# Performance work log

Hardware: AMD Instinct MI355X
Metric: run time of the kernel (lower is better)

## Reference

```python
import jax, jax.numpy as jnp
import numpy as np

# (C,H,W) of x0..x11; flattened size +1 homogeneous coordinate per key
SHAPES = [(3,32,32),(96,32,32),(96,32,32),(96,16,16),(192,16,16),(192,16,16),(192,8,8),(192,8,8),(192,8,8),(640,1,1),(100,1,1),(10,1,1)]
# (Cin,Cout,k,stride,pad) for conv1..conv9
CONV = [(3,96,3,1,1),(96,96,3,1,1),(96,96,3,2,1),(96,192,3,1,1),(192,192,3,1,1),(192,192,3,2,1),(192,192,3,1,1),(192,192,1,1,0),(192,10,1,1,0)]
B = 128


def setup_inputs():
    key = jax.random.key(0)
    inp = {}
    k, key = jax.random.split(key)
    inp['x0'] = jax.random.normal(k, (int(np.prod(SHAPES[0])) + 1, B), jnp.float32)
    for i, s in enumerate(SHAPES):
        n = int(np.prod(s)) + 1
        k1, k2, key = jax.random.split(key, 3)
        inp['perm%d' % i] = jax.random.permutation(k1, n)
        inp['diag%d' % i] = jax.random.uniform(k2, (n,), jnp.float32, 0.5, 1.5)
    for j, (ci, co, ks, st, pd) in enumerate(CONV):
        k1, k2, key = jax.random.split(key, 3)
        inp['w%d' % (j + 1)] = jax.random.normal(k1, (co, ci, ks, ks), jnp.float32) / np.float32(np.sqrt(ci * ks * ks))
        inp['b%d' % (j + 1)] = jax.random.normal(k2, (co,), jnp.float32) * 0.01
    k1, k2, k3, k4 = jax.random.split(key, 4)
    inp['fw1'] = jax.random.normal(k1, (100, 640), jnp.float32) / np.float32(np.sqrt(640))
    inp['fb1'] = jax.random.normal(k2, (100,), jnp.float32) * 0.01
    inp['fw2'] = jax.random.normal(k3, (10, 100), jnp.float32) / np.float32(np.sqrt(100))
    inp['fb2'] = jax.random.normal(k4, (10,), jnp.float32) * 0.01
    return inp


def _decode(x, perm, diag):
    # A_inv @ x with A_inv = P^T D^{-1}; P^T gather index is argsort(perm)
    return (x / diag[:, None])[jnp.argsort(perm)]


def _encode(y, perm, diag):
    # A @ y with A = D P; (P y)[i] = y[perm[i]]
    return diag[:, None] * y[perm]


def _conv_aug(v, w, b, shape_in, stride, pad):
    # affine-augmented conv: [W b; 0 1] applied to [feat; t]
    C, H, Wd = shape_in
    feat, t = v[:-1], v[-1]                      # (C*H*W, B), (B,)
    x = feat.T.reshape(-1, C, H, Wd)
    y = jax.lax.conv_general_dilated(x, w, (stride, stride), [(pad, pad), (pad, pad)],
                                     dimension_numbers=('NCHW', 'OIHW', 'NCHW'))
    y = y + b[None, :, None, None] * t[:, None, None, None]
    yf = y.reshape(y.shape[0], -1).T             # (N_out, B)
    return jnp.concatenate([yf, t[None, :]], axis=0)


def _fc_aug(v, w, b):
    feat, t = v[:-1], v[-1]
    return jnp.concatenate([w @ feat + b[:, None] * t[None, :], t[None, :]], axis=0)


def _forward(x0, perms, diags, ws, bs, fw1, fb1, fw2, fb2):
    x = x0
    for i in range(9):
        v = _decode(x, perms[i], diags[i])
        y = _conv_aug(v, ws[i], bs[i], SHAPES[i], CONV[i][3], CONV[i][4])
        x = jax.nn.relu(_encode(y, perms[i + 1], diags[i + 1]))
    v = _decode(x, perms[9], diags[9])
    x = jax.nn.relu(_encode(_fc_aug(v, fw1, fb1), perms[10], diags[10]))
    v = _decode(x, perms[10], diags[10])
    return _encode(_fc_aug(v, fw2, fb2), perms[11], diags[11])


def reference(x0, perm0, perm1, perm2, perm3, perm4, perm5, perm6, perm7, perm8, perm9, perm10, perm11,
              diag0, diag1, diag2, diag3, diag4, diag5, diag6, diag7, diag8, diag9, diag10, diag11,
              w1, b1, w2, b2, w3, b3, w4, b4, w5, b5, w6, b6, w7, b7, w8, b8, w9, b9,
              fw1, fb1, fw2, fb2):
    perms = [perm0, perm1, perm2, perm3, perm4, perm5, perm6, perm7, perm8, perm9, perm10, perm11]
    diags = [diag0, diag1, diag2, diag3, diag4, diag5, diag6, diag7, diag8, diag9, diag10, diag11]
    ws = [w1, w2, w3, w4, w5, w6, w7, w8, w9]
    bs = [b1, b2, b3, b4, b5, b6, b7, b8, b9]
    return _forward(x0, perms, diags, ws, bs, fw1, fb1, fw2, fb2)
```

## Files before the change

kernel.cpp:

```cpp
#include <hip/hip_runtime.h>
#include <stdint.h>


#define B 128
#define ZPAD 2048
#define NBLK 1024
#define NTHR 256
#define JSTRIDE ((NBLK >> 3) * 4)
#define LEAFN (NBLK >> 3)
#define AGT __HIP_MEMORY_SCOPE_AGENT

typedef _Float16 f16_t;
typedef __attribute__((ext_vector_type(8))) _Float16 f16x8;
typedef __attribute__((ext_vector_type(4))) _Float16 f16x4;
typedef __attribute__((ext_vector_type(4))) float f32x4;

struct WArgs {
    const float* w[9]; const float* b[9];
    int Ci[9], Co[9], KS[9], Cp[9], NCG[9];
    int woff[10]; int boff[10];
};

struct Bufs {
    f16_t *x8in, *S0, *S1, *S2, *S3, *S4, *S5, *S6, *S7, *wp;
    float *bp, *bufA, *bufB, *tph;
    int* bar;
};

__device__ __forceinline__ void st_wt_u64(void* p, uint64_t v) {
    __hip_atomic_store((uint64_t*)p, v, __ATOMIC_RELAXED, AGT);
}
__device__ __forceinline__ void st_wt_u16(void* p, uint16_t v) {
    __hip_atomic_store((uint16_t*)p, v, __ATOMIC_RELAXED, AGT);
}
__device__ __forceinline__ void st_wt_f32(float* p, float v) {
    __hip_atomic_store(p, v, __ATOMIC_RELAXED, AGT);
}
__device__ __forceinline__ void st_wt_h(f16_t* p, f16_t v) {
    union { f16_t h; uint16_t u; } c; c.h = v;
    st_wt_u16(p, c.u);
}

__device__ __forceinline__ void gbar(int* bar, int ph) {
    asm volatile("s_waitcnt vmcnt(0)" ::: "memory");
    __syncthreads();
    if (threadIdx.x == 0) {
        int* leaf  = bar + (blockIdx.x & 7) * 32;
        int* ldone = bar + 256 + (blockIdx.x & 7) * 32;
        int* root  = bar + 512;
        int old = __hip_atomic_fetch_add(leaf, 1, __ATOMIC_RELAXED, AGT);
        if (old == (ph + 1) * LEAFN - 1) {
            __hip_atomic_fetch_add(root, 1, __ATOMIC_RELAXED, AGT);
            while (__hip_atomic_load(root, __ATOMIC_RELAXED, AGT) < (ph + 1) * 8)
                __builtin_amdgcn_s_sleep(8);
            __hip_atomic_store(ldone, ph + 1, __ATOMIC_RELAXED, AGT);
        } else {
            while (__hip_atomic_load(ldone, __ATOMIC_RELAXED, AGT) < ph + 1)
                __builtin_amdgcn_s_sleep(8);
        }
    }
    __syncthreads();
}

__device__ void prep_phase(const WArgs& A, const Bufs& Bf,
                           const float* __restrict__ x0, const int* __restrict__ perm0,
                           const float* __restrict__ diag0) {
    const int NT = NBLK * NTHR;
    const int gtid = blockIdx.x * NTHR + threadIdx.x;
    if (gtid < 512) {
        st_wt_u64((uint64_t*)Bf.x8in + gtid, 0ull);
        st_wt_u64((uint64_t*)Bf.S0 + gtid, 0ull);
        st_wt_u64((uint64_t*)Bf.S1 + gtid, 0ull);
        st_wt_u64((uint64_t*)Bf.S2 + gtid, 0ull);
        st_wt_u64((uint64_t*)Bf.S3 + gtid, 0ull);
        st_wt_u64((uint64_t*)Bf.S4 + gtid, 0ull);
        st_wt_u64((uint64_t*)Bf.S5 + gtid, 0ull);
        st_wt_u64((uint64_t*)Bf.S6 + gtid, 0ull);
        st_wt_u64((uint64_t*)Bf.S7 + gtid, 0ull);
    }
    if (gtid < 1024 * 128) {
        int p = gtid >> 7, n = gtid & 127;
        f16_t* base = Bf.x8in + ZPAD + p * 1024 + n * 8;
        st_wt_u16(base + 3, 0);
        st_wt_u64(base + 4, 0ull);
    }
    if (gtid < A.boff[9]) {
        int l = 0;
        while (gtid >= A.boff[l + 1]) ++l;
        int co = gtid - A.boff[l];
        st_wt_f32(Bf.bp + gtid, (co < A.Co[l]) ? A.b[l][co] : 0.f);
    }
    for (int idx = gtid; idx < A.woff[9]; idx += NT) {
        int l = 0;
        while (idx >= A.woff[l + 1]) ++l;
        int e = idx - A.woff[l];
        int j = e & 7;
        int t1_ = e >> 3;
        int Cp = A.Cp[l];
        int co = t1_ % Cp;
        int gg = t1_ / Cp;
        int ncg = A.NCG[l];
        int tap = gg / ncg, cg = gg - tap * ncg;
        int ks = A.KS[l];
        int kh = tap / ks, kw = tap - kh * ks;
        int ci = cg * 8 + j;
        float val = 0.f;
        if (co < A.Co[l] && tap < ks * ks && ci < A.Ci[l])
            val = A.w[l][(((size_t)co * A.Ci[l] + ci) * ks + kh) * ks + kw];
        st_wt_h(Bf.wp + idx, (f16_t)val);
    }
    for (int idx = gtid; idx < 3073 * B; idx += NT) {
        int row = idx >> 7, n = idx & 127;
        int i = perm0[row];
        float val = x0[(size_t)row * B + n] / diag0[row];
        if (i < 3072) {
            int c = i >> 10, pp = i & 1023;
            st_wt_h(Bf.x8in + ZPAD + pp * 1024 + n * 8 + c, (f16_t)val);
        } else {
            st_wt_f32(Bf.tph + n, val);
        }
    }
}

template <int KS, int NS, int NSPLIT, int CB, bool F32OUT,
          int Hi, int Wo_log2, int HWo, int STRD, int PAD,
          int NCG, int NCHUNK, int KGR, int Co, int Cp>
__device__ __forceinline__ void conv_layer(
    const f16_t* __restrict__ xin, const float* __restrict__ t_in,
    const f16_t* __restrict__ wp, const float* __restrict__ bp,
    f16_t* __restrict__ xout, float* __restrict__ t_out, float* __restrict__ f32out)
{
    constexpr int PF = 2;
    constexpr int MS = 4;
    constexpr int Wi = Hi;
    constexpr int PB8 = HWo / 8;
    constexpr int UJ = NSPLIT * CB * PB8;
    constexpr int HiWi = Hi * Wi;
    constexpr int HiWi4 = 4 * HiWi;
    constexpr int NCGHW = NCG * HiWi;
    const int wv = threadIdx.x >> 6;
    const int lane = threadIdx.x & 63;
    const int q = lane >> 4;
    const int r = lane & 15;
    const int X = blockIdx.x & 7;

    if (blockIdx.x == 0 && threadIdx.x < B) {
        float tvv = fmaxf(t_in[threadIdx.x], 0.f);
        if (F32OUT) st_wt_f32(f32out + (size_t)Co * HWo * B + threadIdx.x, tvv);
        else        st_wt_f32(t_out + threadIdx.x, tvv);
    }

    for (int j = (blockIdx.x >> 3) * 4 + wv; j < UJ; j += JSTRIDE) {
        int nh = 0, j2 = j;
        if (NSPLIT > 1) { nh = j % NSPLIT; j2 = j / NSPLIT; }
        const int cog = (CB > 1) ? (j2 % CB) : 0;
        const int jp  = (CB > 1) ? (j2 / CB) : j2;
        const int p = X * PB8 + jp;
        const int co0 = cog * 64;
        const int ncol0 = nh * (NS * 16);
        const int ncol8 = ncol0 * 8;
        const int ho = p >> Wo_log2;
        const int wo = p & ((1 << Wo_log2) - 1);
        const f16_t* xdata = xin + ZPAD;

        float tv[NS];
#pragma unroll
        for (int ns = 0; ns < NS; ++ns) tv[ns] = t_in[ncol0 + ns * 16 + r];

        f32x4 acc[MS][NS];
#pragma unroll
        for (int ms = 0; ms < MS; ++ms) {
            float4 b4 = *(const float4*)(bp + co0 + ms * 16 + q * 4);
#pragma unroll
            for (int ns = 0; ns < NS; ++ns) {
                acc[ms][ns][0] = b4.x * tv[ns];
                acc[ms][ns][1] = b4.y * tv[ns];
                acc[ms][ns][2] = b4.z * tv[ns];
                acc[ms][ns][3] = b4.w * tv[ns];
            }
        }

        const int hb = ho * STRD - PAD, wb = wo * STRD - PAD;
        const int wend = wb + KS;

        int g = q, cg = q, hi = hb, wi = wb, cgHW;
        {
            while (cg >= NCG) { cg -= NCG; ++wi; if (wi == wend) { wi = wb; ++hi; } }
            cgHW = cg * HiWi;
        }

        f16x8 bf[PF][NS], af[PF][MS];

        auto advance = [&]() {
            g += 4; cg += 4; cgHW += HiWi4;
            if constexpr (NCG >= 4) {
                int c2 = cg - NCG;
                bool wrap = c2 >= 0;
                int wn = wi + 1;
                bool ww = wrap & (wn == wend);
                cg   = wrap ? c2 : cg;
                cgHW = wrap ? cgHW - NCGHW : cgHW;
                wi   = wrap ? (ww ? wb : wn) : wi;
                hi   = ww ? hi + 1 : hi;
            } else {
                while (cg >= NCG) { cg -= NCG; cgHW -= NCGHW; ++wi; if (wi == wend) { wi = wb; ++hi; } }
            }
        };
        auto loadB = [&](f16x8* bb8) {
            bool v = (g < KGR) & ((unsigned)hi < (unsigned)Hi) & ((unsigned)wi < (unsigned)Wi);
            int boff = (cgHW + hi * Wi + wi) << 10;
            const f16_t* bb = xdata + (v ? boff : -ZPAD) + ncol8 + r * 8;
#pragma unroll
            for (int ns = 0; ns < NS; ++ns) bb8[ns] = *(const f16x8*)(bb + ns * 128);
        };
        auto loadA = [&](f16x8* a, int c) {
            int ac = c < NCHUNK ? c : NCHUNK - 1;
            const f16_t* ap = wp + (((ac * 4 + q) * Cp) + co0 + r) * 8;
#pragma unroll
            for (int ms = 0; ms < MS; ++ms) a[ms] = *(const f16x8*)(ap + ms * 128);
        };
        auto domfma = [&](f16x8* a, f16x8* bb8) {
#pragma unroll
            for (int ms = 0; ms < MS; ++ms)
#pragma unroll
                for (int ns = 0; ns < NS; ++ns)
                    acc[ms][ns] = __builtin_amdgcn_mfma_f32_16x16x32_f16(a[ms], bb8[ns], acc[ms][ns], 0, 0, 0);
        };

#pragma unroll
        for (int pf = 0; pf < PF; ++pf) { loadB(bf[pf]); loadA(af[pf], pf); advance(); }
        constexpr int nck = ((NCHUNK + PF - 1) / PF) * PF;
        for (int c = 0; c < nck; c += PF) {
#pragma unroll
            for (int pf = 0; pf < PF; ++pf) {
                domfma(af[pf], bf[pf]);
                loadB(bf[pf]); loadA(af[pf], c + PF + pf); advance();
            }
        }

        if constexpr (!F32OUT) {
#pragma unroll
            for (int ms = 0; ms < MS; ++ms) {
                int cob = co0 + ms * 16 + q * 4;
                if (cob < Co) {
                    int off0 = ((cob >> 3) * HWo + p) * 1024 + (cob & 7) + ncol8 + r * 8;
#pragma unroll
                    for (int ns = 0; ns < NS; ++ns) {
                        union { f16x4 h; uint64_t u; } cu;
                        cu.h[0] = (f16_t)fmaxf(acc[ms][ns][0], 0.f);
                        cu.h[1] = (f16_t)fmaxf(acc[ms][ns][1], 0.f);
                        cu.h[2] = (f16_t)fmaxf(acc[ms][ns][2], 0.f);
                        cu.h[3] = (f16_t)fmaxf(acc[ms][ns][3], 0.f);
                        st_wt_u64(xout + ZPAD + off0 + ns * 128, cu.u);
                    }
                }
            }
        } else {
#pragma unroll
            for (int ms = 0; ms < MS; ++ms)
#pragma unroll
                for (int ns = 0; ns < NS; ++ns)
#pragma unroll
                    for (int e = 0; e < 4; ++e) {
                        int co = co0 + ms * 16 + q * 4 + e;
                        if (co < Co)
                            st_wt_f32(f32out + ((size_t)co * HWo + p) * B + ncol0 + ns * 16 + r,
                                      fmaxf(acc[ms][ns][e], 0.f));
                    }
        }
    }
}

__device__ __forceinline__ void fc1_phase(const float* __restrict__ v, const float* __restrict__ w,
                                          const float* __restrict__ b, float* __restrict__ y,
                                          float* __restrict__ red) {
    int r = blockIdx.x;
    int n = threadIdx.x & 127;
    int kh = threadIdx.x >> 7;
    float t = v[640 * B + n];
    float a0 = 0.f, a1 = 0.f, a2 = 0.f, a3 = 0.f;
    float a4 = 0.f, a5 = 0.f, a6 = 0.f, a7 = 0.f;
    if (r != 100) {
        const float* wr = w + (size_t)r * 640 + kh * 320;
        const float* vr = v + (size_t)kh * 320 * B + n;
        for (int k = 0; k < 320; k += 8) {
            float4 w0 = *(const float4*)(wr + k);
            float4 w1 = *(const float4*)(wr + k + 4);
            a0 = fmaf(w0.x, vr[(k + 0) * B], a0);
            a1 = fmaf(w0.y, vr[(k + 1) * B], a1);
            a2 = fmaf(w0.z, vr[(k + 2) * B], a2);
            a3 = fmaf(w0.w, vr[(k + 3) * B], a3);
            a4 = fmaf(w1.x, vr[(k + 4) * B], a4);
            a5 = fmaf(w1.y, vr[(k + 5) * B], a5);
            a6 = fmaf(w1.z, vr[(k + 6) * B], a6);
            a7 = fmaf(w1.w, vr[(k + 7) * B], a7);
        }
    }
    float part = ((a0 + a1) + (a2 + a3)) + ((a4 + a5) + (a6 + a7));
    if (kh) red[n] = part;
    __syncthreads();
    if (!kh) {
        float val = (r == 100) ? t : b[r] * t + part + red[n];
        st_wt_f32(y + (size_t)r * B + n, fmaxf(val, 0.f));
    }
}

__device__ __forceinline__ void fc2_phase(const float* __restrict__ v, const float* __restrict__ w,
                                          const float* __restrict__ b, const int* __restrict__ perm,
                                          const float* __restrict__ diag, float* __restrict__ out) {
    if (threadIdx.x >= B) return;
    int jrow = blockIdx.x;
    int n = threadIdx.x;
    int r = perm[jrow];
    float d = diag[jrow];
    float t = v[100 * B + n];
    float val;
    if (r == 10) {
        val = t;
    } else {
        float a0 = 0.f, a1 = 0.f, a2 = 0.f, a3 = 0.f;
        const float* wr = w + (size_t)r * 100;
        for (int k = 0; k < 100; k += 4) {
            float4 w4 = *(const float4*)(wr + k);
            a0 = fmaf(w4.x, v[(size_t)(k + 0) * B + n], a0);
            a1 = fmaf(w4.y, v[(size_t)(k + 1) * B + n], a1);
            a2 = fmaf(w4.z, v[(size_t)(k + 2) * B + n], a2);
            a3 = fmaf(w4.w, v[(size_t)(k + 3) * B + n], a3);
        }
        val = b[r] * t + (a0 + a1) + (a2 + a3);
    }
    out[(size_t)jrow * B + n] = d * val;
}

__global__ __launch_bounds__(NTHR, 4) void meganet_kernel(
    WArgs A, Bufs Bf,
    const float* __restrict__ x0, const int* __restrict__ perm0, const float* __restrict__ diag0,
    const int* __restrict__ perm11, const float* __restrict__ diag11,
    const float* __restrict__ fw1, const float* __restrict__ fb1,
    const float* __restrict__ fw2, const float* __restrict__ fb2,
    float* __restrict__ out)
{
    __shared__ float red[128];
    int* bar = Bf.bar;
    float* tp = Bf.tph;

    prep_phase(A, Bf, x0, perm0, diag0);
    gbar(bar, 0);
    conv_layer<3, 2, 4, 2, false, 32, 5, 1024, 1, 1,  1,  3,   9,  96, 128>(
        Bf.x8in, tp, Bf.wp + A.woff[0], Bf.bp + A.boff[0], Bf.S0, tp + 128, nullptr);
    gbar(bar, 1);
    conv_layer<3, 2, 4, 2, false, 32, 5, 1024, 1, 1, 12, 27, 108,  96, 128>(
        Bf.S0, tp + 128, Bf.wp + A.woff[1], Bf.bp + A.boff[1], Bf.S1, tp + 256, nullptr);
    gbar(bar, 2);
    conv_layer<3, 1, 8, 2, false, 32, 4,  256, 2, 1, 12, 27, 108,  96, 128>(
        Bf.S1, tp + 256, Bf.wp + A.woff[2], Bf.bp + A.boff[2], Bf.S2, tp + 384, nullptr);
    gbar(bar, 3);
    conv_layer<3, 2, 4, 3, false, 16, 4,  256, 1, 1, 12, 27, 108, 192, 192>(
        Bf.S2, tp + 384, Bf.wp + A.woff[3], Bf.bp + A.boff[3], Bf.S3, tp + 512, nullptr);
    gbar(bar, 4);
    conv_layer<3, 2, 4, 3, false, 16, 4,  256, 1, 1, 24, 54, 216, 192, 192>(
        Bf.S3, tp + 512, Bf.wp + A.woff[4], Bf.bp + A.boff[4], Bf.S4, tp + 640, nullptr);
    gbar(bar, 5);
    conv_layer<3, 1, 8, 3, false, 16, 3,   64, 2, 1, 24, 54, 216, 192, 192>(
        Bf.S4, tp + 640, Bf.wp + A.woff[5], Bf.bp + A.boff[5], Bf.S5, tp + 768, nullptr);
    gbar(bar, 6);
    conv_layer<3, 1, 8, 3, false,  8, 3,   64, 1, 1, 24, 54, 216, 192, 192>(
        Bf.S5, tp + 768, Bf.wp + A.woff[6], Bf.bp + A.boff[6], Bf.S6, tp + 896, nullptr);
    gbar(bar, 7);
    conv_layer<1, 1, 8, 3, false,  8, 3,   64, 1, 0, 24,  6,  24, 192, 192>(
        Bf.S6, tp + 896, Bf.wp + A.woff[7], Bf.bp + A.boff[7], Bf.S7, tp + 1024, nullptr);
    gbar(bar, 8);
    conv_layer<1, 1, 8, 1, true,   8, 3,   64, 1, 0, 24,  6,  24,  10,  64>(
        Bf.S7, tp + 1024, Bf.wp + A.woff[8], Bf.bp + A.boff[8], nullptr, nullptr, Bf.bufA);
    gbar(bar, 9);
    if (blockIdx.x <= 100) fc1_phase(Bf.bufA, fw1, fb1, Bf.bufB, red);
    gbar(bar, 10);
    if (blockIdx.x < 11) fc2_phase(Bf.bufB, fw2, fb2, perm11, diag11, out);
}


extern "C" void kernel_launch(void* const* d_in, const int* in_sizes, int n_in,
                              void* d_out, int out_size, void* d_ws, size_t ws_size,
                              hipStream_t stream) {
    const float* x0 = (const float*)d_in[0];
    const int*   perm[12];
    const float* diag[12];
    for (int i = 0; i < 12; ++i) {
        perm[i] = (const int*)d_in[1 + 2 * i];
        diag[i] = (const float*)d_in[2 + 2 * i];
    }
    const float* wts[9];
    const float* bia[9];
    for (int j = 0; j < 9; ++j) {
        wts[j] = (const float*)d_in[25 + 2 * j];
        bia[j] = (const float*)d_in[26 + 2 * j];
    }
    const float* fw1 = (const float*)d_in[43];
    const float* fb1 = (const float*)d_in[44];
    const float* fw2 = (const float*)d_in[45];
    const float* fb2 = (const float*)d_in[46];
    float* out = (float*)d_out;

    static const int CiA[9]  = {3, 96, 96, 96, 192, 192, 192, 192, 192};
    static const int CoA[9]  = {96, 96, 96, 192, 192, 192, 192, 192, 10};
    static const int KSA[9]  = {3, 3, 3, 3, 3, 3, 3, 1, 1};
    static const int CpA[9]  = {128, 128, 128, 192, 192, 192, 192, 192, 64};
    static const int NCGA[9] = {1, 12, 12, 12, 24, 24, 24, 24, 24};
    static const int NCHK[9] = {3, 27, 27, 27, 54, 54, 54, 6, 6};

    char* p = (char*)d_ws;
    auto take = [&](size_t bytes) { char* q = p; p += (bytes + 4095) & ~(size_t)4095; return q; };
    Bufs Bf;
    Bf.x8in = (f16_t*)take((ZPAD + 1024 * 1024) * 2);
    Bf.S0   = (f16_t*)take((ZPAD + 12 * 1024 * 1024) * 2);
    Bf.S1   = (f16_t*)take((ZPAD + 12 * 1024 * 1024) * 2);
    Bf.S2   = (f16_t*)take((ZPAD + 3 * 1024 * 1024) * 2);
    Bf.S3   = (f16_t*)take((ZPAD + 6 * 1024 * 1024) * 2);
    Bf.S4   = (f16_t*)take((ZPAD + 6 * 1024 * 1024) * 2);
    Bf.S5   = (f16_t*)take((ZPAD + 1536 * 1024) * 2);
    Bf.S6   = (f16_t*)take((ZPAD + 1536 * 1024) * 2);
    Bf.S7   = (f16_t*)take((ZPAD + 1536 * 1024) * 2);
    Bf.wp   = (f16_t*)take(2888704);
    Bf.bp   = (float*)take(8192);
    Bf.bufA = (float*)take(641 * 128 * 4);
    Bf.bufB = (float*)take(101 * 128 * 4);
    Bf.tph  = (float*)take(10 * 128 * 4);
    Bf.bar  = (int*)  take(4096);

    WArgs WA;
    int wo = 0, bo = 0;
    for (int l = 0; l < 9; ++l) {
        WA.w[l] = wts[l]; WA.b[l] = bia[l];
        WA.Ci[l] = CiA[l]; WA.Co[l] = CoA[l]; WA.KS[l] = KSA[l];
        WA.Cp[l] = CpA[l]; WA.NCG[l] = NCGA[l];
        WA.woff[l] = wo; wo += NCHK[l] * 4 * CpA[l] * 8;
        WA.boff[l] = bo; bo += CpA[l];
    }
    WA.woff[9] = wo; WA.boff[9] = bo;

    hipMemsetAsync(Bf.bar, 0, 4096, stream);

    meganet_kernel<<<NBLK, NTHR, 0, stream>>>(
        WA, Bf, x0, perm[0], diag[0], perm[11], diag[11],
        fw1, fb1, fw2, fb2, out);
}
```

Before: 379.4 us.

## Shrink conv warp tile to one N-subtile and deepen activation prefetch queue

Each wave now computes a 64x16 output tile (NS=1) instead of 64x32 in the layers that used NS=2, with the batch split across 8 wave tasks in every layer. The B-operand loads now run through an 8-deep register ring, and the weight fragments use a separate 2-deep ring, replacing the old 2-stage prefetch. The aim is to keep more global loads in flight and to spread the work across more tasks so latency is hidden better. The cost is that each weight fragment is reused half as much, so more weight loads and more per-task index overhead are issued overall.

```diff
diff --git a/kernel.cpp b/kernel.cpp
--- a/kernel.cpp
+++ b/kernel.cpp
@@ -122,7 +122,7 @@
     }
 }
 
-template <int KS, int NS, int NSPLIT, int CB, bool F32OUT,
+template <int KS, int NSPLIT, int CB, bool F32OUT,
           int Hi, int Wo_log2, int HWo, int STRD, int PAD,
           int NCG, int NCHUNK, int KGR, int Co, int Cp>
 __device__ __forceinline__ void conv_layer(
@@ -130,7 +130,7 @@
     const f16_t* __restrict__ wp, const float* __restrict__ bp,
     f16_t* __restrict__ xout, float* __restrict__ t_out, float* __restrict__ f32out)
 {
-    constexpr int PF = 2;
+    constexpr int BD = 8;
     constexpr int MS = 4;
     constexpr int Wi = Hi;
     constexpr int PB8 = HWo / 8;
@@ -151,33 +151,28 @@
     }
 
     for (int j = (blockIdx.x >> 3) * 4 + wv; j < UJ; j += JSTRIDE) {
-        int nh = 0, j2 = j;
-        if (NSPLIT > 1) { nh = j % NSPLIT; j2 = j / NSPLIT; }
+        const int nh = j % NSPLIT;
+        const int j2 = j / NSPLIT;
         const int cog = (CB > 1) ? (j2 % CB) : 0;
         const int jp  = (CB > 1) ? (j2 / CB) : j2;
         const int p = X * PB8 + jp;
         const int co0 = cog * 64;
-        const int ncol0 = nh * (NS * 16);
+        const int ncol0 = nh * 16;
         const int ncol8 = ncol0 * 8;
         const int ho = p >> Wo_log2;
         const int wo = p & ((1 << Wo_log2) - 1);
         const f16_t* xdata = xin + ZPAD;
 
-        float tv[NS];
-#pragma unroll
-        for (int ns = 0; ns < NS; ++ns) tv[ns] = t_in[ncol0 + ns * 16 + r];
-
-        f32x4 acc[MS][NS];
+        const float tv = t_in[ncol0 + r];
+
+        f32x4 acc[MS];
 #pragma unroll
         for (int ms = 0; ms < MS; ++ms) {
             float4 b4 = *(const float4*)(bp + co0 + ms * 16 + q * 4);
-#pragma unroll
-            for (int ns = 0; ns < NS; ++ns) {
-                acc[ms][ns][0] = b4.x * tv[ns];
-                acc[ms][ns][1] = b4.y * tv[ns];
-                acc[ms][ns][2] = b4.z * tv[ns];
-                acc[ms][ns][3] = b4.w * tv[ns];
-            }
+            acc[ms][0] = b4.x * tv;
+            acc[ms][1] = b4.y * tv;
+            acc[ms][2] = b4.z * tv;
+            acc[ms][3] = b4.w * tv;
         }
 
         const int hb = ho * STRD - PAD, wb = wo * STRD - PAD;
@@ -189,7 +184,7 @@
             cgHW = cg * HiWi;
         }
 
-        f16x8 bf[PF][NS], af[PF][MS];
+        f16x8 bfq[BD], afq[2][MS];
 
         auto advance = [&]() {
             g += 4; cg += 4; cgHW += HiWi4;
@@ -206,12 +201,10 @@
                 while (cg >= NCG) { cg -= NCG; cgHW -= NCGHW; ++wi; if (wi == wend) { wi = wb; ++hi; } }
             }
         };
-        auto loadB = [&](f16x8* bb8) {
+        auto loadB = [&](f16x8& bb8) {
             bool v = (g < KGR) & ((unsigned)hi < (unsigned)Hi) & ((unsigned)wi < (unsigned)Wi);
             int boff = (cgHW + hi * Wi + wi) << 10;
-            const f16_t* bb = xdata + (v ? boff : -ZPAD) + ncol8 + r * 8;
-#pragma unroll
-            for (int ns = 0; ns < NS; ++ns) bb8[ns] = *(const f16x8*)(bb + ns * 128);
+            bb8 = *(const f16x8*)(xdata + (v ? boff : -ZPAD) + ncol8 + r * 8);
         };
         auto loadA = [&](f16x8* a, int c) {
             int ac = c < NCHUNK ? c : NCHUNK - 1;
@@ -219,22 +212,23 @@
 #pragma unroll
             for (int ms = 0; ms < MS; ++ms) a[ms] = *(const f16x8*)(ap + ms * 128);
         };
-        auto domfma = [&](f16x8* a, f16x8* bb8) {
+        auto domfma = [&](f16x8* a, f16x8 bv) {
 #pragma unroll
             for (int ms = 0; ms < MS; ++ms)
-#pragma unroll
-                for (int ns = 0; ns < NS; ++ns)
-                    acc[ms][ns] = __builtin_amdgcn_mfma_f32_16x16x32_f16(a[ms], bb8[ns], acc[ms][ns], 0, 0, 0);
+                acc[ms] = __builtin_amdgcn_mfma_f32_16x16x32_f16(a[ms], bv, acc[ms], 0, 0, 0);
         };
 
 #pragma unroll
-        for (int pf = 0; pf < PF; ++pf) { loadB(bf[pf]); loadA(af[pf], pf); advance(); }
-        constexpr int nck = ((NCHUNK + PF - 1) / PF) * PF;
-        for (int c = 0; c < nck; c += PF) {
-#pragma unroll
-            for (int pf = 0; pf < PF; ++pf) {
-                domfma(af[pf], bf[pf]);
-                loadB(bf[pf]); loadA(af[pf], c + PF + pf); advance();
+        for (int pf = 0; pf < BD; ++pf) { loadB(bfq[pf]); advance(); }
+        loadA(afq[0], 0);
+        loadA(afq[1], 1);
+        constexpr int nck = ((NCHUNK + BD - 1) / BD) * BD;
+        for (int c = 0; c < nck; c += BD) {
+#pragma unroll
+            for (int pf = 0; pf < BD; ++pf) {
+                domfma(afq[pf & 1], bfq[pf]);
+                loadB(bfq[pf]); advance();
+                loadA(afq[pf & 1], c + pf + 2);
             }
         }
 
@@ -244,29 +238,24 @@
                 int cob = co0 + ms * 16 + q * 4;
                 if (cob < Co) {
                     int off0 = ((cob >> 3) * HWo + p) * 1024 + (cob & 7) + ncol8 + r * 8;
-#pragma unroll
-                    for (int ns = 0; ns < NS; ++ns) {
-                        union { f16x4 h; uint64_t u; } cu;
-                        cu.h[0] = (f16_t)fmaxf(acc[ms][ns][0], 0.f);
-                        cu.h[1] = (f16_t)fmaxf(acc[ms][ns][1], 0.f);
-                        cu.h[2] = (f16_t)fmaxf(acc[ms][ns][2], 0.f);
-                        cu.h[3] = (f16_t)fmaxf(acc[ms][ns][3], 0.f);
-                        st_wt_u64(xout + ZPAD + off0 + ns * 128, cu.u);
-                    }
+                    union { f16x4 h; uint64_t u; } cu;
+                    cu.h[0] = (f16_t)fmaxf(acc[ms][0], 0.f);
+                    cu.h[1] = (f16_t)fmaxf(acc[ms][1], 0.f);
+                    cu.h[2] = (f16_t)fmaxf(acc[ms][2], 0.f);
+                    cu.h[3] = (f16_t)fmaxf(acc[ms][3], 0.f);
+                    st_wt_u64(xout + ZPAD + off0, cu.u);
                 }
             }
         } else {
 #pragma unroll
             for (int ms = 0; ms < MS; ++ms)
 #pragma unroll
-                for (int ns = 0; ns < NS; ++ns)
-#pragma unroll
-                    for (int e = 0; e < 4; ++e) {
-                        int co = co0 + ms * 16 + q * 4 + e;
-                        if (co < Co)
-                            st_wt_f32(f32out + ((size_t)co * HWo + p) * B + ncol0 + ns * 16 + r,
-                                      fmaxf(acc[ms][ns][e], 0.f));
-                    }
+                for (int e = 0; e < 4; ++e) {
+                    int co = co0 + ms * 16 + q * 4 + e;
+                    if (co < Co)
+                        st_wt_f32(f32out + ((size_t)co * HWo + p) * B + ncol0 + r,
+                                  fmaxf(acc[ms][e], 0.f));
+                }
         }
     }
 }
@@ -346,31 +335,31 @@
 
     prep_phase(A, Bf, x0, perm0, diag0);
     gbar(bar, 0);
-    conv_layer<3, 2, 4, 2, false, 32, 5, 1024, 1, 1,  1,  3,   9,  96, 128>(
+    conv_layer<3, 8, 2, false, 32, 5, 1024, 1, 1,  1,  3,   9,  96, 128>(
         Bf.x8in, tp, Bf.wp + A.woff[0], Bf.bp + A.boff[0], Bf.S0, tp + 128, nullptr);
     gbar(bar, 1);
-    conv_layer<3, 2, 4, 2, false, 32, 5, 1024, 1, 1, 12, 27, 108,  96, 128>(
+    conv_layer<3, 8, 2, false, 32, 5, 1024, 1, 1, 12, 27, 108,  96, 128>(
         Bf.S0, tp + 128, Bf.wp + A.woff[1], Bf.bp + A.boff[1], Bf.S1, tp + 256, nullptr);
     gbar(bar, 2);
-    conv_layer<3, 1, 8, 2, false, 32, 4,  256, 2, 1, 12, 27, 108,  96, 128>(
+    conv_layer<3, 8, 2, false, 32, 4,  256, 2, 1, 12, 27, 108,  96, 128>(
         Bf.S1, tp + 256, Bf.wp + A.woff[2], Bf.bp + A.boff[2], Bf.S2, tp + 384, nullptr);
     gbar(bar, 3);
-    conv_layer<3, 2, 4, 3, false, 16, 4,  256, 1, 1, 12, 27, 108, 192, 192>(
+    conv_layer<3, 8, 3, false, 16, 4,  256, 1, 1, 12, 27, 108, 192, 192>(
         Bf.S2, tp + 384, Bf.wp + A.woff[3], Bf.bp + A.boff[3], Bf.S3, tp + 512, nullptr);
     gbar(bar, 4);
-    conv_layer<3, 2, 4, 3, false, 16, 4,  256, 1, 1, 24, 54, 216, 192, 192>(
+    conv_layer<3, 8, 3, false, 16, 4,  256, 1, 1, 24, 54, 216, 192, 192>(
         Bf.S3, tp + 512, Bf.wp + A.woff[4], Bf.bp + A.boff[4], Bf.S4, tp + 640, nullptr);
     gbar(bar, 5);
-    conv_layer<3, 1, 8, 3, false, 16, 3,   64, 2, 1, 24, 54, 216, 192, 192>(
+    conv_layer<3, 8, 3, false, 16, 3,   64, 2, 1, 24, 54, 216, 192, 192>(
         Bf.S4, tp + 640, Bf.wp + A.woff[5], Bf.bp + A.boff[5], Bf.S5, tp + 768, nullptr);
     gbar(bar, 6);
-    conv_layer<3, 1, 8, 3, false,  8, 3,   64, 1, 1, 24, 54, 216, 192, 192>(
+    conv_layer<3, 8, 3, false,  8, 3,   64, 1, 1, 24, 54, 216, 192, 192>(
         Bf.S5, tp + 768, Bf.wp + A.woff[6], Bf.bp + A.boff[6], Bf.S6, tp + 896, nullptr);
     gbar(bar, 7);
-    conv_layer<1, 1, 8, 3, false,  8, 3,   64, 1, 0, 24,  6,  24, 192, 192>(
+    conv_layer<1, 8, 3, false,  8, 3,   64, 1, 0, 24,  6,  24, 192, 192>(
         Bf.S6, tp + 896, Bf.wp + A.woff[7], Bf.bp + A.boff[7], Bf.S7, tp + 1024, nullptr);
     gbar(bar, 8);
-    conv_layer<1, 1, 8, 1, true,   8, 3,   64, 1, 0, 24,  6,  24,  10,  64>(
+    conv_layer<1, 8, 1, true,   8, 3,   64, 1, 0, 24,  6,  24,  10,  64>(
         Bf.S7, tp + 1024, Bf.wp + A.woff[8], Bf.bp + A.boff[8], nullptr, nullptr, Bf.bufA);
     gbar(bar, 9);
     if (blockIdx.x <= 100) fc1_phase(Bf.bufA, fw1, fb1, Bf.bufB, red);
```

Result: slower. 468.4 us (+23.5%).

## Group grid barrier by hardware XCC id and use plain cached stores

Applied to the files above, without the earlier changes.

The grid barrier now groups blocks by the XCC id read from a hardware register instead of blockIdx&7, and counts the blocks resident on each XCC at kernel start. It adds a release fence before the root arrive. All intermediate stores change from relaxed agent-scope atomic stores to ordinary stores, which lets writes stay in the per-XCC L2 rather than being forced to device coherence. The risk is cross-XCC visibility: plain stores cached in one XCC's L2 may not be seen by readers on another XCC without a writeback, and the startup counting adds a spin at phase 0.

```diff
diff --git a/kernel.cpp b/kernel.cpp
--- a/kernel.cpp
+++ b/kernel.cpp
@@ -7,7 +7,6 @@
 #define NBLK 1024
 #define NTHR 256
 #define JSTRIDE ((NBLK >> 3) * 4)
-#define LEAFN (NBLK >> 3)
 #define AGT __HIP_MEMORY_SCOPE_AGENT
 
 typedef _Float16 f16_t;
@@ -27,31 +26,41 @@
     int* bar;
 };
 
-__device__ __forceinline__ void st_wt_u64(void* p, uint64_t v) {
-    __hip_atomic_store((uint64_t*)p, v, __ATOMIC_RELAXED, AGT);
-}
-__device__ __forceinline__ void st_wt_u16(void* p, uint16_t v) {
-    __hip_atomic_store((uint16_t*)p, v, __ATOMIC_RELAXED, AGT);
-}
-__device__ __forceinline__ void st_wt_f32(float* p, float v) {
-    __hip_atomic_store(p, v, __ATOMIC_RELAXED, AGT);
-}
-__device__ __forceinline__ void st_wt_h(f16_t* p, f16_t v) {
-    union { f16_t h; uint16_t u; } c; c.h = v;
-    st_wt_u16(p, c.u);
+__device__ __forceinline__ int xcc_id() {
+    int x;
+    asm("s_getreg_b32 %0, hwreg(20, 0, 32)" : "=s"(x));
+    return x & 7;
 }
 
 __device__ __forceinline__ void gbar(int* bar, int ph) {
     asm volatile("s_waitcnt vmcnt(0)" ::: "memory");
     __syncthreads();
     if (threadIdx.x == 0) {
-        int* leaf  = bar + (blockIdx.x & 7) * 32;
-        int* ldone = bar + 256 + (blockIdx.x & 7) * 32;
+        const int x = xcc_id();
+        int* leaf  = bar + x * 32;
+        int* ldone = bar + 256 + x * 32;
         int* root  = bar + 512;
+        int* cnt   = bar + 544;
+        if (ph == 0) {
+            for (;;) {
+                int s = 0;
+#pragma unroll
+                for (int k = 0; k < 8; ++k)
+                    s += __hip_atomic_load(cnt + k, __ATOMIC_RELAXED, AGT);
+                if (s == NBLK) break;
+                __builtin_amdgcn_s_sleep(2);
+            }
+        }
+        const int myc = __hip_atomic_load(cnt + x, __ATOMIC_RELAXED, AGT);
+        int nact = 0;
+#pragma unroll
+        for (int k = 0; k < 8; ++k)
+            nact += (__hip_atomic_load(cnt + k, __ATOMIC_RELAXED, AGT) != 0) ? 1 : 0;
         int old = __hip_atomic_fetch_add(leaf, 1, __ATOMIC_RELAXED, AGT);
-        if (old == (ph + 1) * LEAFN - 1) {
+        if (old == (ph + 1) * myc - 1) {
+            __builtin_amdgcn_fence(__ATOMIC_RELEASE, "agent");
             __hip_atomic_fetch_add(root, 1, __ATOMIC_RELAXED, AGT);
-            while (__hip_atomic_load(root, __ATOMIC_RELAXED, AGT) < (ph + 1) * 8)
+            while (__hip_atomic_load(root, __ATOMIC_RELAXED, AGT) < (ph + 1) * nact)
                 __builtin_amdgcn_s_sleep(8);
             __hip_atomic_store(ldone, ph + 1, __ATOMIC_RELAXED, AGT);
         } else {
@@ -68,27 +77,27 @@
     const int NT = NBLK * NTHR;
     const int gtid = blockIdx.x * NTHR + threadIdx.x;
     if (gtid < 512) {
-        st_wt_u64((uint64_t*)Bf.x8in + gtid, 0ull);
-        st_wt_u64((uint64_t*)Bf.S0 + gtid, 0ull);
-        st_wt_u64((uint64_t*)Bf.S1 + gtid, 0ull);
-        st_wt_u64((uint64_t*)Bf.S2 + gtid, 0ull);
-        st_wt_u64((uint64_t*)Bf.S3 + gtid, 0ull);
-        st_wt_u64((uint64_t*)Bf.S4 + gtid, 0ull);
-        st_wt_u64((uint64_t*)Bf.S5 + gtid, 0ull);
-        st_wt_u64((uint64_t*)Bf.S6 + gtid, 0ull);
-        st_wt_u64((uint64_t*)Bf.S7 + gtid, 0ull);
+        ((uint64_t*)Bf.x8in)[gtid] = 0ull;
+        ((uint64_t*)Bf.S0)[gtid] = 0ull;
+        ((uint64_t*)Bf.S1)[gtid] = 0ull;
+        ((uint64_t*)Bf.S2)[gtid] = 0ull;
+        ((uint64_t*)Bf.S3)[gtid] = 0ull;
+        ((uint64_t*)Bf.S4)[gtid] = 0ull;
+        ((uint64_t*)Bf.S5)[gtid] = 0ull;
+        ((uint64_t*)Bf.S6)[gtid] = 0ull;
+        ((uint64_t*)Bf.S7)[gtid] = 0ull;
     }
     if (gtid < 1024 * 128) {
         int p = gtid >> 7, n = gtid & 127;
         f16_t* base = Bf.x8in + ZPAD + p * 1024 + n * 8;
-        st_wt_u16(base + 3, 0);
-        st_wt_u64(base + 4, 0ull);
+        base[3] = (f16_t)0.f;
+        *(uint64_t*)(base + 4) = 0ull;
     }
     if (gtid < A.boff[9]) {
         int l = 0;
         while (gtid >= A.boff[l + 1]) ++l;
         int co = gtid - A.boff[l];
-        st_wt_f32(Bf.bp + gtid, (co < A.Co[l]) ? A.b[l][co] : 0.f);
+        Bf.bp[gtid] = (co < A.Co[l]) ? A.b[l][co] : 0.f;
     }
     for (int idx = gtid; idx < A.woff[9]; idx += NT) {
         int l = 0;
@@ -107,7 +116,7 @@
         float val = 0.f;
         if (co < A.Co[l] && tap < ks * ks && ci < A.Ci[l])
             val = A.w[l][(((size_t)co * A.Ci[l] + ci) * ks + kh) * ks + kw];
-        st_wt_h(Bf.wp + idx, (f16_t)val);
+        Bf.wp[idx] = (f16_t)val;
     }
     for (int idx = gtid; idx < 3073 * B; idx += NT) {
         int row = idx >> 7, n = idx & 127;
@@ -115,9 +124,9 @@
         float val = x0[(size_t)row * B + n] / diag0[row];
         if (i < 3072) {
             int c = i >> 10, pp = i & 1023;
-            st_wt_h(Bf.x8in + ZPAD + pp * 1024 + n * 8 + c, (f16_t)val);
+            Bf.x8in[ZPAD + pp * 1024 + n * 8 + c] = (f16_t)val;
         } else {
-            st_wt_f32(Bf.tph + n, val);
+            Bf.tph[n] = val;
         }
     }
 }
@@ -146,8 +155,8 @@
 
     if (blockIdx.x == 0 && threadIdx.x < B) {
         float tvv = fmaxf(t_in[threadIdx.x], 0.f);
-        if (F32OUT) st_wt_f32(f32out + (size_t)Co * HWo * B + threadIdx.x, tvv);
-        else        st_wt_f32(t_out + threadIdx.x, tvv);
+        if (F32OUT) f32out[(size_t)Co * HWo * B + threadIdx.x] = tvv;
+        else        t_out[threadIdx.x] = tvv;
     }
 
     for (int j = (blockIdx.x >> 3) * 4 + wv; j < UJ; j += JSTRIDE) {
@@ -246,12 +255,12 @@
                     int off0 = ((cob >> 3) * HWo + p) * 1024 + (cob & 7) + ncol8 + r * 8;
 #pragma unroll
                     for (int ns = 0; ns < NS; ++ns) {
-                        union { f16x4 h; uint64_t u; } cu;
-                        cu.h[0] = (f16_t)fmaxf(acc[ms][ns][0], 0.f);
-                        cu.h[1] = (f16_t)fmaxf(acc[ms][ns][1], 0.f);
-                        cu.h[2] = (f16_t)fmaxf(acc[ms][ns][2], 0.f);
-                        cu.h[3] = (f16_t)fmaxf(acc[ms][ns][3], 0.f);
-                        st_wt_u64(xout + ZPAD + off0 + ns * 128, cu.u);
+                        f16x4 h;
+                        h[0] = (f16_t)fmaxf(acc[ms][ns][0], 0.f);
+                        h[1] = (f16_t)fmaxf(acc[ms][ns][1], 0.f);
+                        h[2] = (f16_t)fmaxf(acc[ms][ns][2], 0.f);
+                        h[3] = (f16_t)fmaxf(acc[ms][ns][3], 0.f);
+                        *(f16x4*)(xout + ZPAD + off0 + ns * 128) = h;
                     }
                 }
             }
@@ -264,8 +273,8 @@
                     for (int e = 0; e < 4; ++e) {
                         int co = co0 + ms * 16 + q * 4 + e;
                         if (co < Co)
-                            st_wt_f32(f32out + ((size_t)co * HWo + p) * B + ncol0 + ns * 16 + r,
-                                      fmaxf(acc[ms][ns][e], 0.f));
+                            f32out[((size_t)co * HWo + p) * B + ncol0 + ns * 16 + r] =
+                                fmaxf(acc[ms][ns][e], 0.f);
                     }
         }
     }
@@ -301,7 +310,7 @@
     __syncthreads();
     if (!kh) {
         float val = (r == 100) ? t : b[r] * t + part + red[n];
-        st_wt_f32(y + (size_t)r * B + n, fmaxf(val, 0.f));
+        y[(size_t)r * B + n] = fmaxf(val, 0.f);
     }
 }
 
@@ -343,6 +352,9 @@
     __shared__ float red[128];
     int* bar = Bf.bar;
     float* tp = Bf.tph;
+
+    if (threadIdx.x == 0)
+        __hip_atomic_fetch_add(bar + 544 + xcc_id(), 1, __ATOMIC_RELAXED, AGT);
 
     prep_phase(A, Bf, x0, perm0, diag0);
     gbar(bar, 0);
```

After: 386.2 us. No clear change (+1.8%).
